# Performance work log

Hardware: AMD Instinct MI355X
Metric: run time of the kernel (lower is better)

The kernel has to match this reference:

```python
import jax, jax.numpy as jnp
import numpy as np

B, N, D = 8, 65536, 192
EPS = 1e-5  # matches cal_norm_batch eps

# corner offsets (i,j,k) in {0,1}^3, shape [2,2,2,3]
_OFFS = np.stack(np.meshgrid(np.arange(2), np.arange(2), np.arange(2), indexing='ij'), -1)


def setup_inputs() -> dict:
    key = jax.random.key(0)
    k1, k2 = jax.random.split(key)
    pss = jax.random.uniform(k1, (B, 3, N), jnp.float32)          # points in [0,1]^3
    sdf_grids = jax.random.normal(k2, (B, D, D, D), jnp.float32)  # per-batch SDF grids
    first = jnp.zeros((B, 3), jnp.float32)                        # grid origin
    coef = jnp.full((B, 3), float(D - 2), jnp.float32)            # 1/voxel_size
    max_limit = jnp.full((B, 3), float(D - 2), jnp.float32)       # keeps idx+1 <= D-1
    return {"pss": pss, "sdf_grids": sdf_grids, "first": first, "coef": coef, "max_limit": max_limit}


def reference(pss, sdf_grids, first, coef, max_limit):
    p = jnp.transpose(pss, (0, 2, 1))  # [B,N,3]
    f_full = jnp.clip(jnp.minimum((p - first[:, None, :]) * coef[:, None, :],
                                  max_limit[:, None, :]), 0.0)
    base = jnp.floor(f_full)
    frac = f_full - base               # [B,N,3] trilinear fractions
    idx8 = base.astype(jnp.int32)[:, :, None, None, None, :] + jnp.asarray(_OFFS, jnp.int32)  # [B,N,2,2,2,3]
    # 8-corner gather, per-batch grid
    corners = jax.vmap(lambda g, I: g[I[..., 0], I[..., 1], I[..., 2]])(sdf_grids, idx8)  # [B,N,2,2,2]
    fx, fy, fz = frac[..., 0], frac[..., 1], frac[..., 2]
    wx = jnp.stack([1 - fx, fx], -1)  # [B,N,2]
    wy = jnp.stack([1 - fy, fy], -1)
    wz = jnp.stack([1 - fz, fz], -1)
    # trilinear SDF value
    dss = jnp.einsum('bnijk,bni,bnj,bnk->bn', corners, wx, wy, wz)
    # finite-difference normals (interp3d_batch with grad=True along each axis)
    n_z = jnp.einsum('bnij,bni,bnj->bn', corners[..., 1] - corners[..., 0], wx, wy)
    n_y = jnp.einsum('bnik,bni,bnk->bn', corners[:, :, :, 1, :] - corners[:, :, :, 0, :], wx, wz)
    n_x = jnp.einsum('bnjk,bnj,bnk->bn', corners[:, :, 1] - corners[:, :, 0], wy, wz)
    n = jnp.stack([n_x, n_y, n_z], -1)  # [B,N,3]
    nss = n / jnp.clip(jnp.linalg.norm(n, axis=-1, keepdims=True), EPS)
    loss = -jnp.sum(jnp.minimum(dss, 0.0))
    return dss, nss, loss
```

## Files before the change

### kernel.cpp

```cpp
#include <hip/hip_runtime.h>

#define BB 8
#define NN 65536
#define DD 192
#define EPSV 1e-5f
#define NPTS (BB * NN)
#define NBLK 1024


__global__ __launch_bounds__(256) void tri_sdf_kernel(
    const float* __restrict__ pss,
    const float* __restrict__ grid,
    const float* __restrict__ first,
    const float* __restrict__ coef,
    const float* __restrict__ maxl,
    float* __restrict__ dss,
    float* __restrict__ nss,
    float* __restrict__ partial)
{
    const int vb = ((int)blockIdx.x & 7) * 128 + ((int)blockIdx.x >> 3);
    const int t0 = vb * 512 + (int)threadIdx.x;
    const int b  = t0 >> 16;
    const int n0 = t0 & (NN - 1);

    const float* pb = pss + (size_t)b * 3 * NN + n0;
    const float pxA = pb[0],        pxB = pb[256];
    const float pyA = pb[NN],       pyB = pb[NN + 256];
    const float pzA = pb[2 * NN],   pzB = pb[2 * NN + 256];

    const float f0x = first[3*b+0], f0y = first[3*b+1], f0z = first[3*b+2];
    const float cfx = coef[3*b+0],  cfy = coef[3*b+1],  cfz = coef[3*b+2];
    const float mlx = maxl[3*b+0],  mly = maxl[3*b+1],  mlz = maxl[3*b+2];

    const float FxA = fmaxf(fminf((pxA - f0x) * cfx, mlx), 0.0f);
    const float FyA = fmaxf(fminf((pyA - f0y) * cfy, mly), 0.0f);
    const float FzA = fmaxf(fminf((pzA - f0z) * cfz, mlz), 0.0f);
    const float FxB = fmaxf(fminf((pxB - f0x) * cfx, mlx), 0.0f);
    const float FyB = fmaxf(fminf((pyB - f0y) * cfy, mly), 0.0f);
    const float FzB = fmaxf(fminf((pzB - f0z) * cfz, mlz), 0.0f);

    const int bxA = (int)floorf(FxA), byA = (int)floorf(FyA), bzA = (int)floorf(FzA);
    const int bxB = (int)floorf(FxB), byB = (int)floorf(FyB), bzB = (int)floorf(FzB);
    const float fxA = FxA - (float)bxA, fyA = FyA - (float)byA, fzA = FzA - (float)bzA;
    const float fxB = FxB - (float)bxB, fyB = FyB - (float)byB, fzB = FzB - (float)bzB;

    const float* gbase = grid + (size_t)b * DD * DD * DD;
    const float* gA = gbase + ((size_t)bxA * DD + byA) * DD + bzA;
    const float* gB = gbase + ((size_t)bxB * DD + byB) * DD + bzB;

    const float a000 = gA[0];
    const float a001 = gA[1];
    const float a010 = gA[DD];
    const float a011 = gA[DD + 1];
    const float a100 = gA[DD * DD];
    const float a101 = gA[DD * DD + 1];
    const float a110 = gA[DD * DD + DD];
    const float a111 = gA[DD * DD + DD + 1];
    const float b000 = gB[0];
    const float b001 = gB[1];
    const float b010 = gB[DD];
    const float b011 = gB[DD + 1];
    const float b100 = gB[DD * DD];
    const float b101 = gB[DD * DD + 1];
    const float b110 = gB[DD * DD + DD];
    const float b111 = gB[DD * DD + DD + 1];

    float wx0 = 1.0f - fxA, wx1 = fxA;
    float wy0 = 1.0f - fyA, wy1 = fyA;
    float wz0 = 1.0f - fzA, wz1 = fzA;

    float d00 = wz0 * a000 + wz1 * a001;
    float d01 = wz0 * a010 + wz1 * a011;
    float d10 = wz0 * a100 + wz1 * a101;
    float d11 = wz0 * a110 + wz1 * a111;
    const float dvA = wx0 * (wy0 * d00 + wy1 * d01) + wx1 * (wy0 * d10 + wy1 * d11);

    const float nzA = wx0 * (wy0 * (a001 - a000) + wy1 * (a011 - a010))
                    + wx1 * (wy0 * (a101 - a100) + wy1 * (a111 - a110));
    const float nyA = wx0 * (wz0 * (a010 - a000) + wz1 * (a011 - a001))
                    + wx1 * (wz0 * (a110 - a100) + wz1 * (a111 - a101));
    const float nxA = wy0 * (wz0 * (a100 - a000) + wz1 * (a101 - a001))
                    + wy1 * (wz0 * (a110 - a010) + wz1 * (a111 - a011));
    const float invA = 1.0f / fmaxf(sqrtf(nxA*nxA + nyA*nyA + nzA*nzA), EPSV);

    wx0 = 1.0f - fxB; wx1 = fxB;
    wy0 = 1.0f - fyB; wy1 = fyB;
    wz0 = 1.0f - fzB; wz1 = fzB;

    d00 = wz0 * b000 + wz1 * b001;
    d01 = wz0 * b010 + wz1 * b011;
    d10 = wz0 * b100 + wz1 * b101;
    d11 = wz0 * b110 + wz1 * b111;
    const float dvB = wx0 * (wy0 * d00 + wy1 * d01) + wx1 * (wy0 * d10 + wy1 * d11);

    const float nzB = wx0 * (wy0 * (b001 - b000) + wy1 * (b011 - b010))
                    + wx1 * (wy0 * (b101 - b100) + wy1 * (b111 - b110));
    const float nyB = wx0 * (wz0 * (b010 - b000) + wz1 * (b011 - b001))
                    + wx1 * (wz0 * (b110 - b100) + wz1 * (b111 - b101));
    const float nxB = wy0 * (wz0 * (b100 - b000) + wz1 * (b101 - b001))
                    + wy1 * (wz0 * (b110 - b010) + wz1 * (b111 - b011));
    const float invB = 1.0f / fmaxf(sqrtf(nxB*nxB + nyB*nyB + nzB*nzB), EPSV);

    dss[t0]       = dvA;
    dss[t0 + 256] = dvB;
    float* npA = nss + (size_t)t0 * 3;
    npA[0] = nxA * invA;
    npA[1] = nyA * invA;
    npA[2] = nzA * invA;
    float* npB = nss + (size_t)(t0 + 256) * 3;
    npB[0] = nxB * invB;
    npB[1] = nyB * invB;
    npB[2] = nzB * invB;

    float lp = fminf(dvA, 0.0f) + fminf(dvB, 0.0f);
    #pragma unroll
    for (int off = 32; off > 0; off >>= 1)
        lp += __shfl_down(lp, off, 64);
    __shared__ float wsum[4];
    const int wid = threadIdx.x >> 6;
    if ((threadIdx.x & 63) == 0) wsum[wid] = lp;
    __syncthreads();
    if (threadIdx.x == 0)
        partial[blockIdx.x] = wsum[0] + wsum[1] + wsum[2] + wsum[3];
}

__global__ __launch_bounds__(256) void loss_reduce_kernel(
    const float* __restrict__ partial, float* __restrict__ loss)
{
    const int tid = threadIdx.x;
    float s = partial[tid] + partial[tid + 256]
            + partial[tid + 512] + partial[tid + 768];
    #pragma unroll
    for (int off = 32; off > 0; off >>= 1)
        s += __shfl_down(s, off, 64);
    __shared__ float wsum[4];
    const int wid = tid >> 6;
    if ((tid & 63) == 0) wsum[wid] = s;
    __syncthreads();
    if (tid == 0)
        loss[0] = -(wsum[0] + wsum[1] + wsum[2] + wsum[3]);
}

extern "C" void kernel_launch(void* const* d_in, const int* in_sizes, int n_in,
                              void* d_out, int out_size, void* d_ws, size_t ws_size,
                              hipStream_t stream) {
    const float* pss   = (const float*)d_in[0];
    const float* grid  = (const float*)d_in[1];
    const float* first = (const float*)d_in[2];
    const float* coef  = (const float*)d_in[3];
    const float* maxl  = (const float*)d_in[4];

    float* out  = (float*)d_out;
    float* dss  = out;
    float* nss  = out + (size_t)BB * NN;
    float* loss = out + (size_t)4 * BB * NN;

    float* partial = (float*)d_ws;

    tri_sdf_kernel<<<NBLK, 256, 0, stream>>>(pss, grid, first, coef, maxl,
                                             dss, nss, partial);
    loss_reduce_kernel<<<1, 256, 0, stream>>>(partial, loss);
}
```

Baseline: 310.3 us.

## Counting-sort points by spatial cell before trilinear gather

Adds a histogram, three-stage prefix scan and scatter pass that bucket points into 8^3-voxel cells per batch, storing each point's scaled coordinate and original index. The main kernel then handles points in sorted order so that nearby points gather nearby grid voxels, aiming for better cache and TLB locality on the large SDF grids. The cost is several extra kernel launches, two reads of the point array, atomics, and output writes to dss and nss that are now scattered rather than coalesced.

```diff
diff --git a/kernel.cpp b/kernel.cpp
--- a/kernel.cpp
+++ b/kernel.cpp
@@ -5,44 +5,126 @@
 #define DD 192
 #define EPSV 1e-5f
 #define NPTS (BB * NN)
-#define NBLK 1024
-
-
-__global__ __launch_bounds__(256) void tri_sdf_kernel(
-    const float* __restrict__ pss,
+
+#define CAX 24
+#define CELLS_B (CAX * CAX * CAX)
+#define TCELLS (BB * CELLS_B)
+#define SCAN_BLOCKS (TCELLS / 256)
+#define MBLK 1024
+
+#define PART0 (TCELLS + 512)
+#define REC0  (PART0 + MBLK)
+
+__device__ __forceinline__ void point_key(
+    const float* __restrict__ pss, const float* __restrict__ first,
+    const float* __restrict__ coef, const float* __restrict__ maxl,
+    int t, float& Fx, float& Fy, float& Fz, int& key)
+{
+    const int b = t >> 16;
+    const int n = t & (NN - 1);
+    const float* pb = pss + (size_t)b * 3 * NN + n;
+    const float px = pb[0];
+    const float py = pb[NN];
+    const float pz = pb[2 * NN];
+
+    Fx = fmaxf(fminf((px - first[3*b+0]) * coef[3*b+0], maxl[3*b+0]), 0.0f);
+    Fy = fmaxf(fminf((py - first[3*b+1]) * coef[3*b+1], maxl[3*b+1]), 0.0f);
+    Fz = fmaxf(fminf((pz - first[3*b+2]) * coef[3*b+2], maxl[3*b+2]), 0.0f);
+
+    const int cx = (int)floorf(Fx) >> 3;
+    const int cy = (int)floorf(Fy) >> 3;
+    const int cz = (int)floorf(Fz) >> 3;
+    key = ((b * CAX + cx) * CAX + cy) * CAX + cz;
+}
+
+__global__ __launch_bounds__(256) void hist_kernel(
+    const float* __restrict__ pss, const float* __restrict__ first,
+    const float* __restrict__ coef, const float* __restrict__ maxl,
+    unsigned* __restrict__ hist)
+{
+    const int vb = ((int)blockIdx.x & 7) * 256 + ((int)blockIdx.x >> 3);
+    const int t  = vb * 256 + (int)threadIdx.x;
+    float Fx, Fy, Fz; int key;
+    point_key(pss, first, coef, maxl, t, Fx, Fy, Fz, key);
+    atomicAdd(&hist[key], 1u);
+}
+
+__global__ __launch_bounds__(256) void scan1_kernel(unsigned* __restrict__ hist,
+                                                    unsigned* __restrict__ bsum)
+{
+    __shared__ unsigned s[256];
+    const int tid = threadIdx.x;
+    const int i = blockIdx.x * 256 + tid;
+    const unsigned v = hist[i];
+    s[tid] = v;
+    __syncthreads();
+    #pragma unroll
+    for (int off = 1; off < 256; off <<= 1) {
+        unsigned tv = (tid >= off) ? s[tid - off] : 0u;
+        __syncthreads();
+        s[tid] += tv;
+        __syncthreads();
+    }
+    hist[i] = s[tid] - v;
+    if (tid == 255) bsum[blockIdx.x] = s[255];
+}
+
+__global__ __launch_bounds__(512) void scan2_kernel(unsigned* __restrict__ bsum)
+{
+    __shared__ unsigned s[512];
+    const int tid = threadIdx.x;
+    const unsigned v = (tid < SCAN_BLOCKS) ? bsum[tid] : 0u;
+    s[tid] = v;
+    __syncthreads();
+    #pragma unroll
+    for (int off = 1; off < 512; off <<= 1) {
+        unsigned tv = (tid >= off) ? s[tid - off] : 0u;
+        __syncthreads();
+        s[tid] += tv;
+        __syncthreads();
+    }
+    if (tid < SCAN_BLOCKS) bsum[tid] = s[tid] - v;
+}
+
+__global__ __launch_bounds__(256) void scan3_kernel(unsigned* __restrict__ hist,
+                                                    const unsigned* __restrict__ bsum)
+{
+    const int i = blockIdx.x * 256 + threadIdx.x;
+    hist[i] += bsum[blockIdx.x];
+}
+
+__global__ __launch_bounds__(256) void scatter_kernel(
+    const float* __restrict__ pss, const float* __restrict__ first,
+    const float* __restrict__ coef, const float* __restrict__ maxl,
+    unsigned* __restrict__ cursor, float4* __restrict__ rec)
+{
+    const int vb = ((int)blockIdx.x & 7) * 256 + ((int)blockIdx.x >> 3);
+    const int t  = vb * 256 + (int)threadIdx.x;
+    float Fx, Fy, Fz; int key;
+    point_key(pss, first, coef, maxl, t, Fx, Fy, Fz, key);
+    const unsigned pos = atomicAdd(&cursor[key], 1u);
+    rec[pos] = make_float4(Fx, Fy, Fz, __uint_as_float((unsigned)t));
+}
+
+__global__ __launch_bounds__(256) void main_kernel(
     const float* __restrict__ grid,
-    const float* __restrict__ first,
-    const float* __restrict__ coef,
-    const float* __restrict__ maxl,
-    float* __restrict__ dss,
-    float* __restrict__ nss,
+    const float4* __restrict__ rec,
+    float* __restrict__ dss, float* __restrict__ nss,
     float* __restrict__ partial)
 {
     const int vb = ((int)blockIdx.x & 7) * 128 + ((int)blockIdx.x >> 3);
-    const int t0 = vb * 512 + (int)threadIdx.x;
-    const int b  = t0 >> 16;
-    const int n0 = t0 & (NN - 1);
-
-    const float* pb = pss + (size_t)b * 3 * NN + n0;
-    const float pxA = pb[0],        pxB = pb[256];
-    const float pyA = pb[NN],       pyB = pb[NN + 256];
-    const float pzA = pb[2 * NN],   pzB = pb[2 * NN + 256];
-
-    const float f0x = first[3*b+0], f0y = first[3*b+1], f0z = first[3*b+2];
-    const float cfx = coef[3*b+0],  cfy = coef[3*b+1],  cfz = coef[3*b+2];
-    const float mlx = maxl[3*b+0],  mly = maxl[3*b+1],  mlz = maxl[3*b+2];
-
-    const float FxA = fmaxf(fminf((pxA - f0x) * cfx, mlx), 0.0f);
-    const float FyA = fmaxf(fminf((pyA - f0y) * cfy, mly), 0.0f);
-    const float FzA = fmaxf(fminf((pzA - f0z) * cfz, mlz), 0.0f);
-    const float FxB = fmaxf(fminf((pxB - f0x) * cfx, mlx), 0.0f);
-    const float FyB = fmaxf(fminf((pyB - f0y) * cfy, mly), 0.0f);
-    const float FzB = fmaxf(fminf((pzB - f0z) * cfz, mlz), 0.0f);
-
-    const int bxA = (int)floorf(FxA), byA = (int)floorf(FyA), bzA = (int)floorf(FzA);
-    const int bxB = (int)floorf(FxB), byB = (int)floorf(FyB), bzB = (int)floorf(FzB);
-    const float fxA = FxA - (float)bxA, fyA = FyA - (float)byA, fzA = FzA - (float)bzA;
-    const float fxB = FxB - (float)bxB, fyB = FyB - (float)byB, fzB = FzB - (float)bzB;
+    const int i0 = vb * 512 + (int)threadIdx.x;
+    const int b  = i0 >> 16;
+
+    const float4 rA = rec[i0];
+    const float4 rB = rec[i0 + 256];
+    const unsigned tA = __float_as_uint(rA.w);
+    const unsigned tB = __float_as_uint(rB.w);
+
+    const int bxA = (int)floorf(rA.x), byA = (int)floorf(rA.y), bzA = (int)floorf(rA.z);
+    const int bxB = (int)floorf(rB.x), byB = (int)floorf(rB.y), bzB = (int)floorf(rB.z);
+    const float fxA = rA.x - (float)bxA, fyA = rA.y - (float)byA, fzA = rA.z - (float)bzA;
+    const float fxB = rB.x - (float)bxB, fyB = rB.y - (float)byB, fzB = rB.z - (float)bzB;
 
     const float* gbase = grid + (size_t)b * DD * DD * DD;
     const float* gA = gbase + ((size_t)bxA * DD + byA) * DD + bzA;
@@ -68,7 +150,6 @@
     float wx0 = 1.0f - fxA, wx1 = fxA;
     float wy0 = 1.0f - fyA, wy1 = fyA;
     float wz0 = 1.0f - fzA, wz1 = fzA;
-
     float d00 = wz0 * a000 + wz1 * a001;
     float d01 = wz0 * a010 + wz1 * a011;
     float d10 = wz0 * a100 + wz1 * a101;
@@ -86,7 +167,6 @@
     wx0 = 1.0f - fxB; wx1 = fxB;
     wy0 = 1.0f - fyB; wy1 = fyB;
     wz0 = 1.0f - fzB; wz1 = fzB;
-
     d00 = wz0 * b000 + wz1 * b001;
     d01 = wz0 * b010 + wz1 * b011;
     d10 = wz0 * b100 + wz1 * b101;
@@ -101,13 +181,13 @@
                     + wy1 * (wz0 * (b110 - b010) + wz1 * (b111 - b011));
     const float invB = 1.0f / fmaxf(sqrtf(nxB*nxB + nyB*nyB + nzB*nzB), EPSV);
 
-    dss[t0]       = dvA;
-    dss[t0 + 256] = dvB;
-    float* npA = nss + (size_t)t0 * 3;
+    dss[tA] = dvA;
+    dss[tB] = dvB;
+    float* npA = nss + (size_t)tA * 3;
     npA[0] = nxA * invA;
     npA[1] = nyA * invA;
     npA[2] = nzA * invA;
-    float* npB = nss + (size_t)(t0 + 256) * 3;
+    float* npB = nss + (size_t)tB * 3;
     npB[0] = nxB * invB;
     npB[1] = nyB * invB;
     npB[2] = nzB * invB;
@@ -155,9 +235,22 @@
     float* nss  = out + (size_t)BB * NN;
     float* loss = out + (size_t)4 * BB * NN;
 
-    float* partial = (float*)d_ws;
-
-    tri_sdf_kernel<<<NBLK, 256, 0, stream>>>(pss, grid, first, coef, maxl,
-                                             dss, nss, partial);
+    unsigned* ws      = (unsigned*)d_ws;
+    unsigned* hist    = ws;
+    unsigned* bsum    = ws + TCELLS;
+    float*    partial = (float*)(ws + PART0);
+    float4*   rec     = (float4*)(ws + REC0);
+
+    hipMemsetAsync(hist, 0, (size_t)TCELLS * sizeof(unsigned), stream);
+
+    const int threads = 256;
+    const int pblocks = NPTS / threads;
+
+    hist_kernel<<<pblocks, threads, 0, stream>>>(pss, first, coef, maxl, hist);
+    scan1_kernel<<<SCAN_BLOCKS, 256, 0, stream>>>(hist, bsum);
+    scan2_kernel<<<1, 512, 0, stream>>>(bsum);
+    scan3_kernel<<<SCAN_BLOCKS, 256, 0, stream>>>(hist, bsum);
+    scatter_kernel<<<pblocks, threads, 0, stream>>>(pss, first, coef, maxl, hist, rec);
+    main_kernel<<<MBLK, 256, 0, stream>>>(grid, rec, dss, nss, partial);
     loss_reduce_kernel<<<1, 256, 0, stream>>>(partial, loss);
 }
```

Measured after the change: 367.3 us. 1.18x slower.
